# Performance work log

Measured on AMD Instinct MI355X. Metric: run time of the kernel, lower is better.

The kernel has to match this reference:

```python
import jax, jax.numpy as jnp
import numpy as np

# PDELayer config (matches torch defaults)
Nx, Ny = 48, 48
Lx, Ly = 1.0, 1.0
T, dt = 0.01, 0.001
dx, dy = Lx / Nx, Ly / Ny
Nt = int(T / dt)  # 10 sequential stencil steps
B = 16384


def setup_inputs() -> dict:
    key = jax.random.key(0)
    u0 = jax.random.normal(key, (B, 1, Nx, Ny), dtype=jnp.float32)
    alpha_w = jnp.array([0.1, 0.1, 0.1], dtype=jnp.float32)  # alpha_w1..3
    beta_w = jnp.array([0.3, 0.2, 0.2], dtype=jnp.float32)   # beta_w1..3
    return {"u0": u0, "alpha_w": alpha_w, "beta_w": beta_w}


def _coeff_grids(alpha_w, beta_w):
    x = jnp.linspace(0.0, Lx, Nx, dtype=jnp.float32)
    y = jnp.linspace(0.0, Ly, Ny, dtype=jnp.float32)
    yy, xx = jnp.meshgrid(y, x, indexing='ij')  # [Ny, Nx]
    two_pi = jnp.float32(2.0 * np.pi)
    alpha_grid = 0.5 * dt * (alpha_w[0]
                             + alpha_w[1] * jnp.sin(two_pi * yy)
                             + alpha_w[2] * jnp.sin(2.0 * two_pi * yy)) / dx ** 2
    beta_grid = dt * (beta_w[0]
                      + beta_w[1] * jnp.cos(two_pi * xx)
                      + beta_w[2] * jnp.cos(2.0 * two_pi * xx)) / dy ** 2
    return alpha_grid[None], beta_grid[None]  # [1, Nx, Ny] (Nx==Ny)


def reference(u0, alpha_w, beta_w):
    alpha_grid, beta_grid = _coeff_grids(alpha_w, beta_w)
    # reflect-pad once; boundary ring stays frozen during time stepping
    u = jnp.pad(u0[:, 0], ((0, 0), (1, 1), (1, 1)), mode='reflect')  # [B, Nx+2, Ny+2]

    def step(u, _):
        ui = u[:, 1:-1, 1:-1]
        u_xx = u[:, 2:, 1:-1] - 2.0 * ui + u[:, :-2, 1:-1]
        u_yy = u[:, 1:-1, 2:] - 2.0 * ui + u[:, 1:-1, :-2]
        u = u.at[:, 1:-1, 1:-1].set(ui + alpha_grid * u_xx + beta_grid * u_yy)
        return u, None

    u, _ = jax.lax.scan(step, u, None, length=Nt)
    return u[:, 1:-1, 1:-1][:, None]  # [B, 1, Nx, Ny]
```

## Files before the change

kernel.cpp:

```cpp
#include <hip/hip_runtime.h>


typedef float v2f __attribute__((ext_vector_type(2)));

constexpr int NXY   = 48;
constexpr int CELLS = NXY * NXY;
constexpr int NT    = 10;
constexpr int TPB   = 64;

__device__ __forceinline__ float dpp_up(float oldv, float src) {
    return __int_as_float(__builtin_amdgcn_update_dpp(
        __float_as_int(oldv), __float_as_int(src), 0x111, 0xF, 0xF, false));
}
__device__ __forceinline__ float dpp_dn(float oldv, float src) {
    return __int_as_float(__builtin_amdgcn_update_dpp(
        __float_as_int(oldv), __float_as_int(src), 0x101, 0xF, 0xF, false));
}

__global__ __launch_bounds__(TPB)
__attribute__((amdgpu_waves_per_eu(2, 3)))
void pde_heat_kernel(
    const float* __restrict__ u0,
    const float* __restrict__ aw,
    const float* __restrict__ bw,
    float* __restrict__ out)
{
    const int lane = threadIdx.x;
    const int r = lane & 15;
    const int c = lane >> 4;
    const long long img0 = (long long)blockIdx.x * 2;
    const float4* __restrict__ u4a = (const float4*)(u0 + img0 * CELLS);
    const float4* __restrict__ u4b = u4a + (CELLS / 4);
    float4*       __restrict__ o4a = (float4*)(out + img0 * CELLS);
    float4*       __restrict__ o4b = o4a + (CELLS / 4);

    const int fb = r * 36 + c * 3;

    v2f A[3][6], B[3][6];
    #pragma unroll
    for (int ii = 0; ii < 3; ++ii)
        #pragma unroll
        for (int k = 0; k < 3; ++k) {
            float4 t = u4a[fb + 12 * ii + k];
            A[ii][2*k]   = (v2f){t.x, t.y};
            A[ii][2*k+1] = (v2f){t.z, t.w};
        }
    #pragma unroll
    for (int ii = 0; ii < 3; ++ii)
        #pragma unroll
        for (int k = 0; k < 3; ++k) {
            float4 t = u4b[fb + 12 * ii + k];
            B[ii][2*k]   = (v2f){t.x, t.y};
            B[ii][2*k+1] = (v2f){t.z, t.w};
        }

    const float a0 = aw[0], a1 = aw[1], a2 = aw[2];
    const float b0 = bw[0], b1 = bw[1], b2 = bw[2];
    float ca[3];
    #pragma unroll
    for (int ii = 0; ii < 3; ++ii) {
        float y = (float)(3 * r + ii) * (1.0f / 47.0f);
        ca[ii] = 1.152f * (a0 + a1 * __builtin_amdgcn_sinf(y)
                              + a2 * __builtin_amdgcn_sinf(2.0f * y));
    }
    v2f cb2[6];
    #pragma unroll
    for (int k = 0; k < 6; ++k) {
        float x0 = (float)(12 * c + 2 * k)     * (1.0f / 47.0f);
        float x1 = (float)(12 * c + 2 * k + 1) * (1.0f / 47.0f);
        cb2[k].x = 2.304f * (b0 + b1 * __builtin_amdgcn_cosf(x0)
                                + b2 * __builtin_amdgcn_cosf(2.0f * x0));
        cb2[k].y = 2.304f * (b0 + b1 * __builtin_amdgcn_cosf(x1)
                                + b2 * __builtin_amdgcn_cosf(2.0f * x1));
    }

    v2f ab[6], hb[6];
    float gH[3], hlp[3], hrp[3];

    const int laneL = lane - 16, laneR = lane + 16;
    const bool cLft = (c == 0), cRgt = (c == 3);

    auto prime = [&](const v2f (&u)[3][6]) {
        #pragma unroll
        for (int k = 0; k < 6; ++k) { ab[k] = u[1][k]; hb[k] = u[1][k]; }
        #pragma unroll
        for (int k = 0; k < 6; ++k) {
            ab[k].x = dpp_up(ab[k].x, u[2][k].x);
            ab[k].y = dpp_up(ab[k].y, u[2][k].y);
            hb[k].x = dpp_dn(hb[k].x, u[0][k].x);
            hb[k].y = dpp_dn(hb[k].y, u[0][k].y);
        }
        #pragma unroll
        for (int ii = 0; ii < 3; ++ii)
            gH[ii] = cLft ? u[ii][0].y : u[ii][5].x;
        #pragma unroll
        for (int ii = 0; ii < 3; ++ii) {
            hlp[ii] = __shfl(u[ii][5].y, laneL);
            hrp[ii] = __shfl(u[ii][0].x, laneR);
        }
    };

    auto cellpair = [&](int ii, int k, const v2f (&rowU)[6], const v2f (&rowM)[6],
                        const v2f (&rowD)[6], float lf, float rt) -> v2f {
        v2f cv = rowM[k];
        v2f s1 = rowU[k] + rowD[k];
        v2f s2;
        s2.x = lf + cv.y;
        s2.y = cv.x + rt;
        v2f uxx = s1 - 2.0f * cv;
        v2f uyy = s2 - 2.0f * cv;
        return cv + ca[ii] * uxx + cb2[k] * uyy;
    };

    auto step = [&](const v2f (&src)[3][6], v2f (&dst)[3][6]) {
        float hl[3], hr[3];
        #pragma unroll
        for (int ii = 0; ii < 3; ++ii) {
            hl[ii] = cLft ? gH[ii] : hlp[ii];
            hr[ii] = cRgt ? gH[ii] : hrp[ii];
        }
        #pragma unroll
        for (int ii = 0; ii < 3; ++ii) {
            const v2f (&rowU)[6] = (ii == 0) ? ab : src[ii - 1];
            const v2f (&rowD)[6] = (ii == 2) ? hb : src[ii + 1];
            #pragma unroll
            for (int k = 1; k < 5; ++k)
                dst[ii][k] = cellpair(ii, k, rowU, src[ii], rowD,
                                      src[ii][k-1].y, src[ii][k+1].x);
            dst[ii][0] = cellpair(ii, 0, rowU, src[ii], rowD,
                                  hl[ii], src[ii][1].x);
            dst[ii][5] = cellpair(ii, 5, rowU, src[ii], rowD,
                                  src[ii][4].y, hr[ii]);
            hlp[ii] = __shfl(dst[ii][5].y, laneL);
            hrp[ii] = __shfl(dst[ii][0].x, laneR);
            if (ii == 2) {
                #pragma unroll
                for (int k = 0; k < 6; ++k) {
                    ab[k].x = dpp_up(ab[k].x, dst[2][k].x);
                    ab[k].y = dpp_up(ab[k].y, dst[2][k].y);
                    hb[k].x = dpp_dn(hb[k].x, dst[0][k].x);
                    hb[k].y = dpp_dn(hb[k].y, dst[0][k].y);
                }
            }
        }
    };

    auto run10 = [&](v2f (&u)[3][6]) {
        #pragma unroll 1
        for (int it = 0; it < NT / 2; ++it) {
            v2f m[3][6];
            step(u, m);
            step(m, u);
        }
    };
    auto storeimg = [&](const v2f (&u)[3][6], float4* __restrict__ o4) {
        #pragma unroll
        for (int ii = 0; ii < 3; ++ii)
            #pragma unroll
            for (int k = 0; k < 3; ++k) {
                float4 t;
                t.x = u[ii][2*k].x;   t.y = u[ii][2*k].y;
                t.z = u[ii][2*k+1].x; t.w = u[ii][2*k+1].y;
                o4[fb + 12 * ii + k] = t;
            }
    };

    prime(A);
    run10(A);
    storeimg(A, o4a);
    prime(B);
    run10(B);
    storeimg(B, o4b);
}

extern "C" void kernel_launch(void* const* d_in, const int* in_sizes, int n_in,
                              void* d_out, int out_size, void* d_ws, size_t ws_size,
                              hipStream_t stream) {
    const float* u0 = (const float*)d_in[0];
    const float* aw = (const float*)d_in[1];
    const float* bw = (const float*)d_in[2];
    float* out = (float*)d_out;

    const int B = in_sizes[0] / CELLS;
    pde_heat_kernel<<<B / 2, TPB, 0, stream>>>(u0, aw, bw, out);
}
```

Baseline: 82.26 us.

## Interleave time steps of both images per block to hide DPP/shuffle latency

Each thread now carries its own halo state for both images and alternates stencil steps between image A and image B in one loop, rather than fully processing A before B. The goal is to give the scheduler independent work to fill DPP and cross-lane shuffle latency, and to overlap B's compute with A's memory phases. Waves-per-EU is capped at 2 so the extra live registers fit. The cost is more VGPR pressure, possibly lower occupancy, and the risk of spills.

Result: slower. 84.46 us (+2.7%).

```diff
diff --git a/kernel.cpp b/kernel.cpp
--- a/kernel.cpp
+++ b/kernel.cpp
@@ -18,7 +18,7 @@
 }
 
 __global__ __launch_bounds__(TPB)
-__attribute__((amdgpu_waves_per_eu(2, 3)))
+__attribute__((amdgpu_waves_per_eu(2, 2)))
 void pde_heat_kernel(
     const float* __restrict__ u0,
     const float* __restrict__ aw,
@@ -74,13 +74,14 @@
                                 + b2 * __builtin_amdgcn_cosf(2.0f * x1));
     }
 
-    v2f ab[6], hb[6];
-    float gH[3], hlp[3], hrp[3];
-
     const int laneL = lane - 16, laneR = lane + 16;
     const bool cLft = (c == 0), cRgt = (c == 3);
 
-    auto prime = [&](const v2f (&u)[3][6]) {
+    v2f abA[6], hbA[6], abB[6], hbB[6];
+    float gHA[3], hlpA[3], hrpA[3], gHB[3], hlpB[3], hrpB[3];
+
+    auto prime = [&](const v2f (&u)[3][6], v2f (&ab)[6], v2f (&hb)[6],
+                     float (&gH)[3], float (&hlp)[3], float (&hrp)[3]) {
         #pragma unroll
         for (int k = 0; k < 6; ++k) { ab[k] = u[1][k]; hb[k] = u[1][k]; }
         #pragma unroll
@@ -112,7 +113,9 @@
         return cv + ca[ii] * uxx + cb2[k] * uyy;
     };
 
-    auto step = [&](const v2f (&src)[3][6], v2f (&dst)[3][6]) {
+    auto step = [&](const v2f (&src)[3][6], v2f (&dst)[3][6],
+                    v2f (&ab)[6], v2f (&hb)[6], const float (&gH)[3],
+                    float (&hlp)[3], float (&hrp)[3]) {
         float hl[3], hr[3];
         #pragma unroll
         for (int ii = 0; ii < 3; ++ii) {
@@ -145,32 +148,36 @@
         }
     };
 
-    auto run10 = [&](v2f (&u)[3][6]) {
-        #pragma unroll 1
-        for (int it = 0; it < NT / 2; ++it) {
-            v2f m[3][6];
-            step(u, m);
-            step(m, u);
+    prime(A, abA, hbA, gHA, hlpA, hrpA);
+    prime(B, abB, hbB, gHB, hlpB, hrpB);
+
+    #pragma unroll 1
+    for (int it = 0; it < NT / 2; ++it) {
+        v2f mA[3][6], mB[3][6];
+        step(A,  mA, abA, hbA, gHA, hlpA, hrpA);
+        step(B,  mB, abB, hbB, gHB, hlpB, hrpB);
+        step(mA, A,  abA, hbA, gHA, hlpA, hrpA);
+        step(mB, B,  abB, hbB, gHB, hlpB, hrpB);
+    }
+
+    #pragma unroll
+    for (int ii = 0; ii < 3; ++ii)
+        #pragma unroll
+        for (int k = 0; k < 3; ++k) {
+            float4 t;
+            t.x = A[ii][2*k].x;   t.y = A[ii][2*k].y;
+            t.z = A[ii][2*k+1].x; t.w = A[ii][2*k+1].y;
+            o4a[fb + 12 * ii + k] = t;
         }
-    };
-    auto storeimg = [&](const v2f (&u)[3][6], float4* __restrict__ o4) {
+    #pragma unroll
+    for (int ii = 0; ii < 3; ++ii)
         #pragma unroll
-        for (int ii = 0; ii < 3; ++ii)
-            #pragma unroll
-            for (int k = 0; k < 3; ++k) {
-                float4 t;
-                t.x = u[ii][2*k].x;   t.y = u[ii][2*k].y;
-                t.z = u[ii][2*k+1].x; t.w = u[ii][2*k+1].y;
-                o4[fb + 12 * ii + k] = t;
-            }
-    };
-
-    prime(A);
-    run10(A);
-    storeimg(A, o4a);
-    prime(B);
-    run10(B);
-    storeimg(B, o4b);
+        for (int k = 0; k < 3; ++k) {
+            float4 t;
+            t.x = B[ii][2*k].x;   t.y = B[ii][2*k].y;
+            t.z = B[ii][2*k+1].x; t.w = B[ii][2*k+1].y;
+            o4b[fb + 12 * ii + k] = t;
+        }
 }
 
 extern "C" void kernel_launch(void* const* d_in, const int* in_sizes, int n_in,
```
